# Optimization experiments

Measured on AMD Instinct MI355X. Metric: run time of the kernel, lower is better.

The kernel has to match this reference:

```python
import jax, jax.numpy as jnp
import numpy as np

B, S, Nv, D, DF, H = 8, 1024, 768, 512, 2048, 8
DH = D // H
EPS = 1e-5


def _layernorm(x, g, b):
    mu = jnp.mean(x, axis=-1, keepdims=True)
    var = jnp.mean((x - mu) ** 2, axis=-1, keepdims=True)
    return (x - mu) * jax.lax.rsqrt(var + EPS) * g + b


def _mha(x, Wq, Wk, Wv, Wo):
    b, s, d = x.shape
    q = (x @ Wq).reshape(b, s, H, DH)
    k = (x @ Wk).reshape(b, s, H, DH)
    v = (x @ Wv).reshape(b, s, H, DH)
    scores = jnp.einsum('bqhd,bkhd->bhqk', q, k) / np.sqrt(DH).astype(np.float32)
    a = jax.nn.softmax(scores, axis=-1)
    o = jnp.einsum('bhqk,bkhd->bqhd', a, v).reshape(b, s, d)
    return o @ Wo


def setup_inputs() -> dict:
    key = jax.random.key(0)
    ks = jax.random.split(key, 20)
    sc = 1.0 / np.sqrt(D)
    scf = 1.0 / np.sqrt(DF)
    n = lambda k, shp, s: (jax.random.normal(k, shp, jnp.float32) * s)
    return {
        'x': n(ks[0], (B, S, D), 1.0),
        'idx_emb_1': jax.random.randint(ks[1], (B, Nv), 0, Nv, dtype=jnp.int64) if jax.config.jax_enable_x64 else jax.random.randint(ks[1], (B, Nv), 0, Nv).astype(jnp.int32),
        'idx_pro_1': jax.random.randint(ks[2], (B, Nv), 0, Nv).astype(jnp.int32),
        'N': Nv,
        'Wq1': n(ks[3], (D, D), sc), 'Wk1': n(ks[4], (D, D), sc),
        'Wv1': n(ks[5], (D, D), sc), 'Wo1': n(ks[6], (D, D), sc),
        'Wq2': n(ks[7], (D, D), sc), 'Wk2': n(ks[8], (D, D), sc),
        'Wv2': n(ks[9], (D, D), sc), 'Wo2': n(ks[10], (D, D), sc),
        'w_conv1': n(ks[11], (D, DF), sc), 'b_conv1': jnp.zeros((DF,), jnp.float32),
        'w_conv2': n(ks[12], (DF, D), scf), 'b_conv2': jnp.zeros((D,), jnp.float32),
        'g1': jnp.ones((D,), jnp.float32), 'beta1': jnp.zeros((D,), jnp.float32),
        'g2': jnp.ones((D,), jnp.float32), 'beta2': jnp.zeros((D,), jnp.float32),
    }


def reference(x, idx_emb_1, idx_pro_1, N,
              Wq1, Wk1, Wv1, Wo1, Wq2, Wk2, Wv2, Wo2,
              w_conv1, b_conv1, w_conv2, b_conv2, g1, beta1, g2, beta2):
    # batched gather-reorder of first N tokens; rest pass through
    x_l1 = x.at[:, :N].set(jnp.take_along_axis(x[:, :N], idx_emb_1[:, :, None].astype(jnp.int32), axis=1))
    attn1 = _mha(x_l1, Wq1, Wk1, Wv1, Wo1)
    attn2 = jnp.flip(_mha(jnp.flip(x_l1, axis=1), Wq2, Wk2, Wv2, Wo2), axis=1)
    new_x1 = attn1 + attn2
    x_l2 = new_x1.at[:, :N].set(jnp.take_along_axis(new_x1[:, :N], idx_pro_1[:, :, None].astype(jnp.int32), axis=1))
    x = _layernorm(x + x_l2, g1, beta1)
    # kernel-size-1 Conv1d FFN == pointwise linear (dropout=0, eval mode)
    y = jnp.maximum(x @ w_conv1 + b_conv1, 0.0)
    y = y @ w_conv2 + b_conv2
    out = _layernorm(x + y, g2, beta2)
    return (out, attn1, attn2)
```

## Files before the change

kernel.cpp:

```cpp
#include <hip/hip_runtime.h>
#include <hip/hip_bf16.h>
#include <stdint.h>

#define B_ 8
#define S_ 1024
#define NV_ 768
#define D_ 512
#define DF_ 2048
#define H_ 8
#define DH_ 64
#define BS_ (B_*S_)
#define BSD_ ((size_t)B_*S_*D_)
#define QKLD 2048

typedef __bf16 bf16x8 __attribute__((ext_vector_type(8)));
typedef float f32x4 __attribute__((ext_vector_type(4)));
typedef float f32x16 __attribute__((ext_vector_type(16)));
typedef __hip_bfloat16 bf16;

__device__ __forceinline__ void async_copy16(const void* g, void* l) {
  __builtin_amdgcn_global_load_lds((const __attribute__((address_space(1))) void*)g,
                                   (__attribute__((address_space(3))) void*)l, 16, 0, 0);
}

template<int NT>
__device__ __forceinline__ void stage_tile(const bf16* __restrict__ g, int gRow0, long ldg,
                                           int gCol0, bf16* lds, int rows, int tid) {
  const int totalBytes = rows << 7;
  for (int off = tid * 16; off < totalBytes; off += NT * 16) {
    const int r = off >> 7;
    const int c = off & 127;
    const int srcByte = c ^ ((r & 7) << 4);
    const bf16* gp = g + (long)(gRow0 + r) * ldg + gCol0 + (srcByte >> 1);
    async_copy16(gp, (char*)lds + off);
  }
}
__device__ __forceinline__ bf16x8 lds_frag(const bf16* base, int row, int kElem) {
  const int byte = (row << 7) + ((kElem << 1) ^ ((row & 7) << 4));
  return *(const bf16x8*)((const char*)base + byte);
}

__device__ __forceinline__ int fswz(int row) {
  return ((((row >> 3) & 3) << 1) | (row & 1)) << 4;
}

#define SCH_BIAS 1064872540.f
template<int BASE>
__device__ __forceinline__ bf16x8 pexp_frag(const f32x16& s) {
  union { unsigned u[4]; bf16x8 b; } r;
#pragma unroll
  for (int e = 0; e < 4; e++) {
    const int i0 = (int)fmaf(s[BASE + 2 * e], 8388608.f, SCH_BIAS);
    const int i1 = (int)fmaf(s[BASE + 2 * e + 1], 8388608.f, SCH_BIAS);
    r.u[e] = __builtin_amdgcn_perm((unsigned)i1, (unsigned)i0, 0x07060302u);
  }
  return r.b;
}

__device__ __forceinline__ bf16x8 ones_frag() {
  union { ushort u[8]; bf16x8 b; } r;
#pragma unroll
  for (int e = 0; e < 8; e++) r.u[e] = 0x3F80;
  return r.b;
}

__device__ __forceinline__ f32x16 zero16() {
  f32x16 z;
#pragma unroll
  for (int i = 0; i < 16; i++) z[i] = 0.f;
  return z;
}

struct WPanel { const float* src; bf16* dst; int srcLd, dstLd; float scale; };
struct WP16 { WPanel p[16]; };
__global__ __launch_bounds__(256) void wtrans16_kernel(WP16 ws) {
  __shared__ float tile[32][33];
  const WPanel pa = ws.p[blockIdx.z];
  const int tx = threadIdx.x, ty = threadIdx.y;
  const int n0 = blockIdx.x * 32, k0 = blockIdx.y * 32;
#pragma unroll
  for (int i = 0; i < 4; i++)
    tile[ty + i * 8][tx] = pa.src[(long)(k0 + ty + i * 8) * pa.srcLd + n0 + tx];
  __syncthreads();
#pragma unroll
  for (int i = 0; i < 4; i++)
    pa.dst[(long)(n0 + ty + i * 8) * pa.dstLd + k0 + tx] =
        __float2bfloat16(tile[tx][ty + i * 8] * pa.scale);
}

__global__ __launch_bounds__(256) void gather_cvt_kernel(const float* __restrict__ x,
                                                         const int* __restrict__ idx,
                                                         const int* __restrict__ Np,
                                                         bf16* __restrict__ out) {
  const int N = *Np;
  const int row = blockIdx.x * 2 + (threadIdx.x >> 7);
  const int t = threadIdx.x & 127;
  const int b = row >> 10, s = row & 1023;
  const int src = (s < N) ? idx[b * NV_ + s] : s;
  const float4 v = *(const float4*)(x + ((long)b * S_ + src) * D_ + t * 4);
  ushort4 u;
  u.x = (ushort)__bfloat16_as_ushort(__float2bfloat16(v.x));
  u.y = (ushort)__bfloat16_as_ushort(__float2bfloat16(v.y));
  u.z = (ushort)__bfloat16_as_ushort(__float2bfloat16(v.z));
  u.w = (ushort)__bfloat16_as_ushort(__float2bfloat16(v.w));
  *(ushort4*)(out + (long)row * D_ + t * 4) = u;
}

template<int BM, int BN, int MR, int NR, int OUTF, int BIAS, int RELU, int QKV>
__global__ __launch_bounds__(BM / (MR * 16) * (BN / (NR * 16)) * 64)
void gemm_bt(const bf16* __restrict__ A, long lda, long sAz,
             const bf16* __restrict__ Bt, long sBz,
             const float* __restrict__ bias,
             void* __restrict__ C, long ldc, long sCz,
             int K, bf16* __restrict__ vtbOut) {
  constexpr int WC = BN / (NR * 16);
  constexpr int WR = BM / (MR * 16);
  constexpr int NT = WR * WC * 64;
  __shared__ bf16 As[BM * 64];
  __shared__ bf16 Bs[BN * 64];
  const int tid = threadIdx.x;
  const int lane = tid & 63, wave = tid >> 6;
  const int wr = wave / WC, wc = wave % WC;
  const int g = lane >> 4, lr = lane & 15;

  const int nx = gridDim.x;
  const int ch = nx >> 3;
  const int l = blockIdx.x + nx * blockIdx.y;
  const int xcd = l & 7, i = l >> 3;
  const int bx = xcd * ch + i % ch;
  const int by = i / ch;
  const int m0 = bx * BM, n0 = by * BN;
  const int z = blockIdx.z;
  A += (long)z * sAz;
  Bt += (long)z * sBz;

  f32x4 acc[MR][NR];
#pragma unroll
  for (int m = 0; m < MR; m++)
#pragma unroll
    for (int n = 0; n < NR; n++) acc[m][n] = (f32x4){0.f, 0.f, 0.f, 0.f};

  for (int kt = 0; kt < K; kt += 64) {
    stage_tile<NT>(A, m0, lda, kt, As, BM, tid);
    stage_tile<NT>(Bt, n0, K, kt, Bs, BN, tid);
    __syncthreads();
#pragma unroll
    for (int ks = 0; ks < 64; ks += 32) {
      const int kk = ks + g * 8;
      bf16x8 aF[MR], bF[NR];
#pragma unroll
      for (int m = 0; m < MR; m++) aF[m] = lds_frag(As, wr * (MR * 16) + m * 16 + lr, kk);
#pragma unroll
      for (int n = 0; n < NR; n++) bF[n] = lds_frag(Bs, wc * (NR * 16) + n * 16 + lr, kk);
#pragma unroll
      for (int m = 0; m < MR; m++)
#pragma unroll
        for (int n = 0; n < NR; n++)
          acc[m][n] = __builtin_amdgcn_mfma_f32_16x16x32_bf16(aF[m], bF[n], acc[m][n], 0, 0, 0);
    }
    __syncthreads();
  }

#pragma unroll
  for (int m = 0; m < MR; m++) {
#pragma unroll
    for (int n = 0; n < NR; n++) {
      const int row = m0 + wr * (MR * 16) + m * 16 + g * 4;
      const int col = n0 + wc * (NR * 16) + n * 16 + lr;
      if (QKV) {
        const int set = (col >= 1536) ? 1 : 0;
        const int c1 = col - set * 1536;
        if (c1 < 1024) {
          bf16* cp = (bf16*)C + (long)row * QKLD + set * 1024 + c1;
#pragma unroll
          for (int r = 0; r < 4; r++) cp[(long)r * QKLD] = __float2bfloat16(acc[m][n][r]);
        } else {
          const int d = c1 - 1024;
          const int zz = set * 64 + ((row >> 10) << 3) + (d >> 6);
          const int s = row & 1023;
          const int sp = (s & ~12) | ((s & 4) << 1) | ((s & 8) >> 1);
          ushort4 pk;
          pk.x = (ushort)__bfloat16_as_ushort(__float2bfloat16(acc[m][n][0]));
          pk.y = (ushort)__bfloat16_as_ushort(__float2bfloat16(acc[m][n][1]));
          pk.z = (ushort)__bfloat16_as_ushort(__float2bfloat16(acc[m][n][2]));
          pk.w = (ushort)__bfloat16_as_ushort(__float2bfloat16(acc[m][n][3]));
          *(ushort4*)(vtbOut + (((long)(zz * 64 + (d & 63))) << 10) + sp) = pk;
        }
      } else {
        const float bv = BIAS ? bias[col] : 0.f;
#pragma unroll
        for (int r = 0; r < 4; r++) {
          float v = acc[m][n][r] + bv;
          if (RELU) v = fmaxf(v, 0.f);
          if (OUTF) ((float*)C)[(long)z * sCz + (long)(row + r) * ldc + col] = v;
          else ((bf16*)C)[(long)z * sCz + (long)(row + r) * ldc + col] = __float2bfloat16(v);
        }
      }
    }
  }
}

__global__ __launch_bounds__(256, 2) void flash_kernel(bf16* __restrict__ qk,
                                                       const bf16* __restrict__ vtb) {
  __shared__ char lds[32768];
  const int tid = threadIdx.x;
  const int lane = tid & 63, warp = tid >> 6;
  const int qlo = lane & 31, hi = lane >> 5;

  const int bid = (int)blockIdx.x;
  const int swz = (bid & 7) * 64 + (bid >> 3);
  const int qt = swz & 3;
  const int sbh = swz >> 2;
  const int set = sbh >> 6;
  const int b = (sbh >> 3) & 7, h = sbh & 7;

  bf16* Qp = qk + (long)b * S_ * QKLD + set * 1024 + h * DH_;
  const bf16* Kp = Qp + 512;
  const bf16* Vp = vtb + (long)sbh * DH_ * S_;

  const int r0 = tid >> 3;
  const int cbyt = (tid & 7) << 4;
  const int sb = cbyt ^ fswz(r0);
  char* const ld0 = lds + tid * 16;

  {
    const bf16* qS = Qp + (long)(qt * 256 + r0) * QKLD + (sb >> 1);
#pragma unroll
    for (int i = 0; i < 8; i++) async_copy16(qS + (long)i * 32 * QKLD, ld0 + i * 4096);
  }
  __syncthreads();

  const int qrow = warp * 32 + qlo;
  const int qrb = (qrow << 7) | fswz(qrow);
  bf16x8 qA[4], qB[4];
#pragma unroll
  for (int d4 = 0; d4 < 4; d4++) {
    const int kc2 = d4 * 32 + hi * 16;
    qA[d4] = *(const bf16x8*)(lds + (qrb ^ kc2));
    qB[d4] = *(const bf16x8*)(lds + ((qrb + 16384) ^ kc2));
  }
  __syncthreads();

  const bf16* kS = Kp + (long)r0 * QKLD + (sb >> 1);
  const bf16* vS = Vp + (long)r0 * S_ + (sb >> 1);
  async_copy16(kS, ld0);
  async_copy16(kS + 32 * QKLD, ld0 + 4096);
  async_copy16(vS, ld0 + 8192);
  async_copy16(vS + 32 * S_, ld0 + 12288);
  __syncthreads();
  kS += 64 * QKLD; vS += 64;
  async_copy16(kS, ld0 + 16384);
  async_copy16(kS + 32 * QKLD, ld0 + 16384 + 4096);
  async_copy16(vS, ld0 + 16384 + 8192);
  async_copy16(vS + 32 * S_, ld0 + 16384 + 12288);

  f32x16 oA0 = zero16(), oA1 = zero16(), sAccA = zero16();
  f32x16 oB0 = zero16(), oB1 = zero16(), sAccB = zero16();
  const bf16x8 onesF = ones_frag();
  const int rb = (qlo << 7) | fswz(qlo);

#pragma unroll 1
  for (int t = 0; t < 16; t++) {
    const int cbase = (t & 1) << 14;
    const int kbase = cbase + rb;
    const int vbase = cbase + 8192 + rb;

    f32x16 sA0 = zero16(), sA1 = zero16(), sB0 = zero16(), sB1 = zero16();
    __builtin_amdgcn_s_setprio(1);
#pragma unroll
    for (int d4 = 0; d4 < 4; d4++) {
      const int kc2 = d4 * 32 + hi * 16;
      const bf16x8 kf0 = *(const bf16x8*)(lds + (kbase ^ kc2));
      const bf16x8 kf1 = *(const bf16x8*)(lds + ((kbase + 4096) ^ kc2));
      sA0 = __builtin_amdgcn_mfma_f32_32x32x16_bf16(kf0, qA[d4], sA0, 0, 0, 0);
      sA1 = __builtin_amdgcn_mfma_f32_32x32x16_bf16(kf1, qA[d4], sA1, 0, 0, 0);
      sB0 = __builtin_amdgcn_mfma_f32_32x32x16_bf16(kf0, qB[d4], sB0, 0, 0, 0);
      sB1 = __builtin_amdgcn_mfma_f32_32x32x16_bf16(kf1, qB[d4], sB1, 0, 0, 0);
    }

#pragma unroll
    for (int ks = 0; ks < 4; ks++) {
      bf16x8 paA, paB;
      if (ks == 0)      { paA = pexp_frag<0>(sA0); paB = pexp_frag<0>(sB0); }
      else if (ks == 1) { paA = pexp_frag<8>(sA0); paB = pexp_frag<8>(sB0); }
      else if (ks == 2) { paA = pexp_frag<0>(sA1); paB = pexp_frag<0>(sB1); }
      else              { paA = pexp_frag<8>(sA1); paB = pexp_frag<8>(sB1); }
      const int off = ks * 32 + hi * 16;
      const bf16x8 v0 = *(const bf16x8*)(lds + (vbase ^ off));
      const bf16x8 v1 = *(const bf16x8*)(lds + ((vbase + 4096) ^ off));
      oA0 = __builtin_amdgcn_mfma_f32_32x32x16_bf16(paA, v0, oA0, 0, 0, 0);
      oA1 = __builtin_amdgcn_mfma_f32_32x32x16_bf16(paA, v1, oA1, 0, 0, 0);
      sAccA = __builtin_amdgcn_mfma_f32_32x32x16_bf16(paA, onesF, sAccA, 0, 0, 0);
      oB0 = __builtin_amdgcn_mfma_f32_32x32x16_bf16(paB, v0, oB0, 0, 0, 0);
      oB1 = __builtin_amdgcn_mfma_f32_32x32x16_bf16(paB, v1, oB1, 0, 0, 0);
      sAccB = __builtin_amdgcn_mfma_f32_32x32x16_bf16(paB, onesF, sAccB, 0, 0, 0);
    }
    __builtin_amdgcn_s_setprio(0);

    __syncthreads();
    if (t + 2 < 16) {
      kS += 64 * QKLD; vS += 64;
      char* dst = ld0 + cbase;
      async_copy16(kS, dst);
      async_copy16(kS + 32 * QKLD, dst + 4096);
      async_copy16(vS, dst + 8192);
      async_copy16(vS + 32 * S_, dst + 12288);
    }
  }

#pragma unroll
  for (int r = 0; r < 16; r++) {
    const int q = (r & 3) + 8 * (r >> 2) + 4 * hi;
    bf16* opA = Qp + (long)(qt * 256 + warp * 32 + q) * QKLD;
    bf16* opB = opA + (long)128 * QKLD;
    const float liA = 1.f / sAccA[r];
    const float liB = 1.f / sAccB[r];
    opA[qlo] = __float2bfloat16(oA0[r] * liA);
    opA[32 + qlo] = __float2bfloat16(oA1[r] * liA);
    opB[qlo] = __float2bfloat16(oB0[r] * liB);
    opB[32 + qlo] = __float2bfloat16(oB1[r] * liB);
  }
}

__global__ __launch_bounds__(256) void fuse1_kernel(const float* __restrict__ x,
                                                    const float* __restrict__ a1,
                                                    const float* __restrict__ a2,
                                                    const int* __restrict__ idx,
                                                    const int* __restrict__ Np,
                                                    const float* __restrict__ gw,
                                                    const float* __restrict__ bw,
                                                    bf16* __restrict__ xlnB) {
  const int N = *Np;
  const int row = blockIdx.x * 4 + (threadIdx.x >> 6);
  const int lane = threadIdx.x & 63;
  const int b = row >> 10, s = row & 1023;
  const int j = (s < N) ? idx[b * NV_ + s] : s;
  const float* xp = x + (long)row * D_ + lane * 8;
  const float* p1 = a1 + ((long)b * S_ + j) * D_ + lane * 8;
  const float* p2 = a2 + ((long)b * S_ + j) * D_ + lane * 8;
  float v[8];
  float sum = 0.f;
#pragma unroll
  for (int q = 0; q < 2; q++) {
    const float4 t = ((const float4*)xp)[q];
    const float4 u = ((const float4*)p1)[q];
    const float4 w = ((const float4*)p2)[q];
    v[q * 4 + 0] = t.x + u.x + w.x; v[q * 4 + 1] = t.y + u.y + w.y;
    v[q * 4 + 2] = t.z + u.z + w.z; v[q * 4 + 3] = t.w + u.w + w.w;
  }
#pragma unroll
  for (int i = 0; i < 8; i++) sum += v[i];
#pragma unroll
  for (int o = 1; o < 64; o <<= 1) sum += __shfl_xor(sum, o, 64);
  const float mu = sum * (1.f / D_);
  float var = 0.f;
#pragma unroll
  for (int i = 0; i < 8; i++) { const float t = v[i] - mu; var += t * t; }
#pragma unroll
  for (int o = 1; o < 64; o <<= 1) var += __shfl_xor(var, o, 64);
  const float rs = rsqrtf(var * (1.f / D_) + 1e-5f);
#pragma unroll
  for (int i = 0; i < 8; i++) {
    const int d = lane * 8 + i;
    xlnB[(long)row * D_ + d] = __float2bfloat16((v[i] - mu) * rs * gw[d] + bw[d]);
  }
}

__global__ __launch_bounds__(256) void fuse2_kernel(const bf16* __restrict__ xlnB,
                                                    const bf16* __restrict__ ybf,
                                                    const float* __restrict__ gw,
                                                    const float* __restrict__ bw,
                                                    float* __restrict__ out) {
  const int row = blockIdx.x * 4 + (threadIdx.x >> 6);
  const int lane = threadIdx.x & 63;
  const bf16* xp = xlnB + (long)row * D_ + lane * 8;
  const bf16* yp = ybf + (long)row * D_ + lane * 8;
  float v[8];
  float sum = 0.f;
#pragma unroll
  for (int i = 0; i < 8; i++) {
    v[i] = __bfloat162float(xp[i]) + __bfloat162float(yp[i]);
    sum += v[i];
  }
#pragma unroll
  for (int o = 1; o < 64; o <<= 1) sum += __shfl_xor(sum, o, 64);
  const float mu = sum * (1.f / D_);
  float var = 0.f;
#pragma unroll
  for (int i = 0; i < 8; i++) { const float t = v[i] - mu; var += t * t; }
#pragma unroll
  for (int o = 1; o < 64; o <<= 1) var += __shfl_xor(var, o, 64);
  const float rs = rsqrtf(var * (1.f / D_) + 1e-5f);
#pragma unroll
  for (int i = 0; i < 8; i++) {
    const int d = lane * 8 + i;
    out[(long)row * D_ + d] = (v[i] - mu) * rs * gw[d] + bw[d];
  }
}

extern "C" void kernel_launch(void* const* d_in, const int* in_sizes, int n_in,
                              void* d_out, int out_size, void* d_ws, size_t ws_size,
                              hipStream_t stream) {
  const float* x   = (const float*)d_in[0];
  const int* idx1  = (const int*)d_in[1];
  const int* idx2  = (const int*)d_in[2];
  const int* Np    = (const int*)d_in[3];
  const float* b_conv1 = (const float*)d_in[13];
  const float* b_conv2 = (const float*)d_in[15];
  const float* g1    = (const float*)d_in[16];
  const float* beta1 = (const float*)d_in[17];
  const float* g2    = (const float*)d_in[18];
  const float* beta2 = (const float*)d_in[19];

  float* outp  = (float*)d_out;
  float* attn1 = outp + BSD_;

  const size_t DD = (size_t)D_ * D_;
  char* w = (char*)d_ws;
  bf16* wT  = (bf16*)w;
  bf16* w1T = wT + 8 * DD;
  bf16* w2T = w1T + (size_t)DF_ * D_;
  bf16* qk  = (bf16*)(w + (8ll << 20));
  bf16* xl1 = (bf16*)(w + (40ll << 20));
  bf16* xlnB = (bf16*)(w + (48ll << 20));
  bf16* vtb = (bf16*)(w + (56ll << 20));
  bf16* ffn = qk;
  bf16* ybf = xl1;

  WP16 wp;
  const float* attnW[8] = {(const float*)d_in[4], (const float*)d_in[5], (const float*)d_in[6],
                           (const float*)d_in[8], (const float*)d_in[9], (const float*)d_in[10],
                           (const float*)d_in[7], (const float*)d_in[11]};
  for (int z = 0; z < 8; z++) {
    wp.p[z].src = attnW[z];
    wp.p[z].dst = wT + (size_t)z * DD;
    wp.p[z].srcLd = D_; wp.p[z].dstLd = D_;
    wp.p[z].scale = (z == 0 || z == 3) ? 0.1803368801f : 1.f;
  }
  for (int j = 0; j < 4; j++) {
    wp.p[8 + j].src = (const float*)d_in[12] + 512 * j;
    wp.p[8 + j].dst = w1T + (size_t)(512 * j) * D_;
    wp.p[8 + j].srcLd = DF_; wp.p[8 + j].dstLd = D_;
    wp.p[8 + j].scale = 1.f;
  }
  for (int j = 0; j < 4; j++) {
    wp.p[12 + j].src = (const float*)d_in[14] + (size_t)(512 * j) * D_;
    wp.p[12 + j].dst = w2T + 512 * j;
    wp.p[12 + j].srcLd = D_; wp.p[12 + j].dstLd = DF_;
    wp.p[12 + j].scale = 1.f;
  }

  const dim3 tb(32, 8);
  wtrans16_kernel<<<dim3(16, 16, 16), tb, 0, stream>>>(wp);

  gather_cvt_kernel<<<BS_ / 2, 256, 0, stream>>>(x, idx1, Np, xl1);

  gemm_bt<128, 128, 4, 4, 0, 0, 0, 1><<<dim3(BS_ / 128, 3072 / 128, 1), 256, 0, stream>>>(
      xl1, D_, 0, wT, 0, nullptr, qk, QKLD, 0, D_, vtb);

  flash_kernel<<<512, 256, 0, stream>>>(qk, vtb);

  gemm_bt<128, 128, 4, 4, 1, 0, 0, 0><<<dim3(BS_ / 128, D_ / 128, 2), 256, 0, stream>>>(
      qk, QKLD, 1024, wT + 6 * DD, (long)DD, nullptr, attn1, D_, (long)BSD_, D_, nullptr);

  fuse1_kernel<<<BS_ / 4, 256, 0, stream>>>(x, attn1, attn1 + BSD_, idx2, Np, g1, beta1, xlnB);

  gemm_bt<128, 128, 4, 4, 0, 1, 1, 0><<<dim3(BS_ / 128, DF_ / 128, 1), 256, 0, stream>>>(
      xlnB, D_, 0, w1T, 0, b_conv1, ffn, DF_, 0, D_, nullptr);
  gemm_bt<128, 64, 4, 2, 0, 1, 0, 0><<<dim3(BS_ / 128, D_ / 64, 1), 256, 0, stream>>>(
      ffn, DF_, 0, w2T, 0, b_conv2, ybf, D_, 0, DF_, nullptr);

  fuse2_kernel<<<BS_ / 4, 256, 0, stream>>>(xlnB, ybf, g2, beta2, outp);
}
```

Baseline: 186.5 us.

## Add 256x256 double-buffered GEMM kernel for QKV and FFN1 projections

Introduces a 512-thread GEMM with 256x256 output tiles, double-buffered LDS staging of 64-wide K slices, and an XCD-aware block swizzle. It is used for the QKV projection and the first FFN GEMM in place of the 128x128 kernel. The epilogue is factored into a shared store helper. Larger tiles raise operand reuse per LDS load, but they give fewer blocks (256 for QKV) and higher register and LDS pressure at one block per CU.

```diff
diff --git a/kernel.cpp b/kernel.cpp
--- a/kernel.cpp
+++ b/kernel.cpp
@@ -69,6 +69,42 @@
 #pragma unroll
   for (int i = 0; i < 16; i++) z[i] = 0.f;
   return z;
+}
+
+template<int OUTF, int BIAS, int RELU, int QKV>
+__device__ __forceinline__ void gemm_store(const f32x4& a, int row, int col,
+                                           const float* __restrict__ bias,
+                                           void* __restrict__ C, long ldc, long sCz, int z,
+                                           bf16* __restrict__ vtbOut) {
+  if (QKV) {
+    const int set = (col >= 1536) ? 1 : 0;
+    const int c1 = col - set * 1536;
+    if (c1 < 1024) {
+      bf16* cp = (bf16*)C + (long)row * QKLD + set * 1024 + c1;
+#pragma unroll
+      for (int r = 0; r < 4; r++) cp[(long)r * QKLD] = __float2bfloat16(a[r]);
+    } else {
+      const int d = c1 - 1024;
+      const int zz = set * 64 + ((row >> 10) << 3) + (d >> 6);
+      const int s = row & 1023;
+      const int sp = (s & ~12) | ((s & 4) << 1) | ((s & 8) >> 1);
+      ushort4 pk;
+      pk.x = (ushort)__bfloat16_as_ushort(__float2bfloat16(a[0]));
+      pk.y = (ushort)__bfloat16_as_ushort(__float2bfloat16(a[1]));
+      pk.z = (ushort)__bfloat16_as_ushort(__float2bfloat16(a[2]));
+      pk.w = (ushort)__bfloat16_as_ushort(__float2bfloat16(a[3]));
+      *(ushort4*)(vtbOut + (((long)(zz * 64 + (d & 63))) << 10) + sp) = pk;
+    }
+  } else {
+    const float bv = BIAS ? bias[col] : 0.f;
+#pragma unroll
+    for (int r = 0; r < 4; r++) {
+      float v = a[r] + bv;
+      if (RELU) v = fmaxf(v, 0.f);
+      if (OUTF) ((float*)C)[(long)z * sCz + (long)(row + r) * ldc + col] = v;
+      else ((bf16*)C)[(long)z * sCz + (long)(row + r) * ldc + col] = __float2bfloat16(v);
+    }
+  }
 }
 
 struct WPanel { const float* src; bf16* dst; int srcLd, dstLd; float scale; };
@@ -162,42 +198,85 @@
   }
 
 #pragma unroll
-  for (int m = 0; m < MR; m++) {
-#pragma unroll
-    for (int n = 0; n < NR; n++) {
-      const int row = m0 + wr * (MR * 16) + m * 16 + g * 4;
-      const int col = n0 + wc * (NR * 16) + n * 16 + lr;
-      if (QKV) {
-        const int set = (col >= 1536) ? 1 : 0;
-        const int c1 = col - set * 1536;
-        if (c1 < 1024) {
-          bf16* cp = (bf16*)C + (long)row * QKLD + set * 1024 + c1;
-#pragma unroll
-          for (int r = 0; r < 4; r++) cp[(long)r * QKLD] = __float2bfloat16(acc[m][n][r]);
-        } else {
-          const int d = c1 - 1024;
-          const int zz = set * 64 + ((row >> 10) << 3) + (d >> 6);
-          const int s = row & 1023;
-          const int sp = (s & ~12) | ((s & 4) << 1) | ((s & 8) >> 1);
-          ushort4 pk;
-          pk.x = (ushort)__bfloat16_as_ushort(__float2bfloat16(acc[m][n][0]));
-          pk.y = (ushort)__bfloat16_as_ushort(__float2bfloat16(acc[m][n][1]));
-          pk.z = (ushort)__bfloat16_as_ushort(__float2bfloat16(acc[m][n][2]));
-          pk.w = (ushort)__bfloat16_as_ushort(__float2bfloat16(acc[m][n][3]));
-          *(ushort4*)(vtbOut + (((long)(zz * 64 + (d & 63))) << 10) + sp) = pk;
-        }
-      } else {
-        const float bv = BIAS ? bias[col] : 0.f;
-#pragma unroll
-        for (int r = 0; r < 4; r++) {
-          float v = acc[m][n][r] + bv;
-          if (RELU) v = fmaxf(v, 0.f);
-          if (OUTF) ((float*)C)[(long)z * sCz + (long)(row + r) * ldc + col] = v;
-          else ((bf16*)C)[(long)z * sCz + (long)(row + r) * ldc + col] = __float2bfloat16(v);
-        }
-      }
-    }
-  }
+  for (int m = 0; m < MR; m++)
+#pragma unroll
+    for (int n = 0; n < NR; n++)
+      gemm_store<OUTF, BIAS, RELU, QKV>(acc[m][n], m0 + wr * (MR * 16) + m * 16 + g * 4,
+                                        n0 + wc * (NR * 16) + n * 16 + lr,
+                                        bias, C, ldc, sCz, z, vtbOut);
+}
+
+template<int OUTF, int BIAS, int RELU, int QKV>
+__global__ __launch_bounds__(512, 1)
+void gemm_big(const bf16* __restrict__ A, long lda,
+              const bf16* __restrict__ Bt,
+              const float* __restrict__ bias,
+              void* __restrict__ C, long ldc,
+              int K, bf16* __restrict__ vtbOut) {
+  constexpr int BM = 256, BN = 256, MR = 8, NR = 4;
+  constexpr int WC = 4, WR = 2, NT = 512;
+  __shared__ bf16 As[2][BM * 64];
+  __shared__ bf16 Bs[2][BN * 64];
+  const int tid = threadIdx.x;
+  const int lane = tid & 63, wave = tid >> 6;
+  const int wr = wave / WC, wc = wave % WC;
+  const int g = lane >> 4, lr = lane & 15;
+
+  const int nx = gridDim.x;
+  const int ch = nx >> 3;
+  const int l = blockIdx.x + nx * blockIdx.y;
+  const int xcd = l & 7, i = l >> 3;
+  const int bx = xcd * ch + i % ch;
+  const int by = i / ch;
+  const int m0 = bx * BM, n0 = by * BN;
+
+  f32x4 acc[MR][NR];
+#pragma unroll
+  for (int m = 0; m < MR; m++)
+#pragma unroll
+    for (int n = 0; n < NR; n++) acc[m][n] = (f32x4){0.f, 0.f, 0.f, 0.f};
+
+  const int nk = K >> 6;
+  stage_tile<NT>(A, m0, lda, 0, As[0], BM, tid);
+  stage_tile<NT>(Bt, n0, K, 0, Bs[0], BN, tid);
+  __syncthreads();
+  if (nk > 1) {
+    stage_tile<NT>(A, m0, lda, 64, As[1], BM, tid);
+    stage_tile<NT>(Bt, n0, K, 64, Bs[1], BN, tid);
+  }
+
+#pragma unroll 1
+  for (int t = 0; t < nk; t++) {
+    const bf16* Acur = As[t & 1];
+    const bf16* Bcur = Bs[t & 1];
+#pragma unroll
+    for (int ks = 0; ks < 64; ks += 32) {
+      const int kk = ks + g * 8;
+      bf16x8 aF[MR], bF[NR];
+#pragma unroll
+      for (int m = 0; m < MR; m++) aF[m] = lds_frag(Acur, wr * (MR * 16) + m * 16 + lr, kk);
+#pragma unroll
+      for (int n = 0; n < NR; n++) bF[n] = lds_frag(Bcur, wc * (NR * 16) + n * 16 + lr, kk);
+#pragma unroll
+      for (int m = 0; m < MR; m++)
+#pragma unroll
+        for (int n = 0; n < NR; n++)
+          acc[m][n] = __builtin_amdgcn_mfma_f32_16x16x32_bf16(aF[m], bF[n], acc[m][n], 0, 0, 0);
+    }
+    __syncthreads();
+    if (t + 2 < nk) {
+      stage_tile<NT>(A, m0, lda, (t + 2) << 6, (bf16*)As[t & 1], BM, tid);
+      stage_tile<NT>(Bt, n0, K, (t + 2) << 6, (bf16*)Bs[t & 1], BN, tid);
+    }
+  }
+
+#pragma unroll
+  for (int m = 0; m < MR; m++)
+#pragma unroll
+    for (int n = 0; n < NR; n++)
+      gemm_store<OUTF, BIAS, RELU, QKV>(acc[m][n], m0 + wr * (MR * 16) + m * 16 + g * 4,
+                                        n0 + wc * (NR * 16) + n * 16 + lr,
+                                        bias, C, ldc, 0, 0, vtbOut);
 }
 
 __global__ __launch_bounds__(256, 2) void flash_kernel(bf16* __restrict__ qk,
@@ -455,8 +534,8 @@
 
   gather_cvt_kernel<<<BS_ / 2, 256, 0, stream>>>(x, idx1, Np, xl1);
 
-  gemm_bt<128, 128, 4, 4, 0, 0, 0, 1><<<dim3(BS_ / 128, 3072 / 128, 1), 256, 0, stream>>>(
-      xl1, D_, 0, wT, 0, nullptr, qk, QKLD, 0, D_, vtb);
+  gemm_big<0, 0, 0, 1><<<dim3(BS_ / 256, 3072 / 256), 512, 0, stream>>>(
+      xl1, D_, wT, nullptr, qk, QKLD, D_, vtb);
 
   flash_kernel<<<512, 256, 0, stream>>>(qk, vtb);
 
@@ -465,8 +544,8 @@
 
   fuse1_kernel<<<BS_ / 4, 256, 0, stream>>>(x, attn1, attn1 + BSD_, idx2, Np, g1, beta1, xlnB);
 
-  gemm_bt<128, 128, 4, 4, 0, 1, 1, 0><<<dim3(BS_ / 128, DF_ / 128, 1), 256, 0, stream>>>(
-      xlnB, D_, 0, w1T, 0, b_conv1, ffn, DF_, 0, D_, nullptr);
+  gemm_big<0, 1, 1, 0><<<dim3(BS_ / 256, DF_ / 256), 512, 0, stream>>>(
+      xlnB, D_, w1T, b_conv1, ffn, DF_, D_, nullptr);
   gemm_bt<128, 64, 4, 2, 0, 1, 0, 0><<<dim3(BS_ / 128, D_ / 64, 1), 256, 0, stream>>>(
       ffn, DF_, 0, w2T, 0, b_conv2, ybf, D_, 0, DF_, nullptr);
 
```

Result: slower. 192.9 us (+3.4%).
